# Optimization experiments

Hardware: AMD Instinct MI355X
Metric: run time of the kernel (lower is better)

The kernel has to match this reference:

```python
import jax, jax.numpy as jnp
import numpy as np
jax.config.update('jax_enable_x64', True)

H = 16          # tree height -> n = 2**H
TP = 16         # parallel coordinate dims
F = 2
DIV = 2
K = F * H // DIV          # 16
N = 1 << H                # 65536
EMB = 1_000_000
T = 2048                  # rows in this block


def setup_inputs() -> dict:
    key = jax.random.key(0)
    k1, k2, k3 = jax.random.split(key, 3)
    # location table: signed ints in [1-n, n), as in torch.randint(1-n, n, ...)
    locations = jax.random.randint(k1, (EMB, TP), 1 - N, N, dtype=jnp.int64)
    pos_idx = jax.random.randint(k2, (T,), 0, EMB, dtype=jnp.int64)
    norm = jax.random.uniform(k3, (T, 1, 1), dtype=jnp.float32)
    return {"locations": locations, "pos_idx": pos_idx, "norm": norm}


def _generate_random_masks(key, sz):
    # masks[i] uniform in [0, 2**i) per level i  (note: & binds looser than -,
    # so torch code computes rand & (2**i - 1))
    upper = (jnp.int64(1) << jnp.arange(H, dtype=jnp.int64)) - 1  # (H,)
    rn = jax.random.randint(key, (H, sz, K, TP), 0, N, dtype=jnp.int64)
    masks = rn & upper[:, None, None, None]
    return jnp.transpose(masks, (1, 0, 2, 3))  # (sz, H, K, TP)


def _connection(key, ori_int):
    # ori_int: (T, TP) int64
    kmask, kperm = jax.random.split(key)
    flip_masks = (jnp.int64(1) << jnp.arange(H, dtype=jnp.int64))[None, :, None]  # (1,H,1)
    flipped = ori_int[:, None, :] ^ flip_masks                    # (T, H, TP)
    rmasks = _generate_random_masks(kmask, flipped.shape[0])      # (T, H, K, TP)
    result = (flipped[:, :, None, :] ^ rmasks).reshape(T, H * K, TP)
    loc = jnp.concatenate([result, ori_int[:, None, :], -result], axis=1)  # (T, 2HK+1, TP)
    perm = jax.random.permutation(kperm, loc.shape[1])
    return loc[:, perm, :]


def _distance(coord1, coord2, norm):
    # sign product: +1 if same sign (>=0 vs <0), else -1
    sg = (jnp.where(coord1 >= 0, 1.0, -1.0) * jnp.where(coord2 >= 0, 1.0, -1.0)).astype(jnp.float32)
    xor = jnp.abs(coord1) ^ jnp.abs(coord2)
    _, e = jnp.frexp((xor + 1).astype(jnp.float32))  # frexp exponent == bit length
    s = e.astype(jnp.float32) / H
    return sg * (1.0 - s) * norm


def reference(locations, pos_idx, norm):
    # gather this block's node locations (irregular gather from large table)
    ori = locations[pos_idx]                         # (T, TP)
    key = jax.random.key(42)
    loc = _connection(key, ori)                      # (T, 2HK+1, TP) candidate neighbors
    # distances from each candidate back to the original location
    return _distance(loc, ori[:, None, :], norm)     # (T, 2HK+1, TP) float32
```

## Files before the change

### kernel.cpp

```cpp
#include <hip/hip_runtime.h>
#include <stdint.h>


#define H_   16
#define TP_  16
#define K_   16
#define T_   2048
#define NC   513

typedef float f32x4 __attribute__((ext_vector_type(4)));

struct TFPair { uint32_t a, b; };

__host__ __device__ constexpr uint32_t rotl32(uint32_t x, int r) {
  return (x << r) | (x >> (32 - r));
}

__host__ __device__ constexpr TFPair tf2x32(uint32_t k0, uint32_t k1,
                                            uint32_t x0, uint32_t x1) {
  uint32_t ks0 = k0, ks1 = k1, ks2 = k0 ^ k1 ^ 0x1BD11BDAu;
  x0 += ks0; x1 += ks1;
  x0 += x1; x1 = rotl32(x1, 13); x1 ^= x0;
  x0 += x1; x1 = rotl32(x1, 15); x1 ^= x0;
  x0 += x1; x1 = rotl32(x1, 26); x1 ^= x0;
  x0 += x1; x1 = rotl32(x1,  6); x1 ^= x0;
  x0 += ks1; x1 += ks2 + 1u;
  x0 += x1; x1 = rotl32(x1, 17); x1 ^= x0;
  x0 += x1; x1 = rotl32(x1, 29); x1 ^= x0;
  x0 += x1; x1 = rotl32(x1, 16); x1 ^= x0;
  x0 += x1; x1 = rotl32(x1, 24); x1 ^= x0;
  x0 += ks2; x1 += ks0 + 2u;
  x0 += x1; x1 = rotl32(x1, 13); x1 ^= x0;
  x0 += x1; x1 = rotl32(x1, 15); x1 ^= x0;
  x0 += x1; x1 = rotl32(x1, 26); x1 ^= x0;
  x0 += x1; x1 = rotl32(x1,  6); x1 ^= x0;
  x0 += ks0; x1 += ks1 + 3u;
  x0 += x1; x1 = rotl32(x1, 17); x1 ^= x0;
  x0 += x1; x1 = rotl32(x1, 29); x1 ^= x0;
  x0 += x1; x1 = rotl32(x1, 16); x1 ^= x0;
  x0 += x1; x1 = rotl32(x1, 24); x1 ^= x0;
  x0 += ks1; x1 += ks2 + 4u;
  x0 += x1; x1 = rotl32(x1, 13); x1 ^= x0;
  x0 += x1; x1 = rotl32(x1, 15); x1 ^= x0;
  x0 += x1; x1 = rotl32(x1, 26); x1 ^= x0;
  x0 += x1; x1 = rotl32(x1,  6); x1 ^= x0;
  x0 += ks2; x1 += ks0 + 5u;
  return {x0, x1};
}

constexpr TFPair KM = tf2x32(0u, 42u, 0u, 0u);
constexpr TFPair KP = tf2x32(0u, 42u, 0u, 1u);
constexpr TFPair C2 = tf2x32(KM.a, KM.b, 0u, 1u);
constexpr uint32_t KLO0 = C2.a, KLO1 = C2.b;
constexpr TFPair SB = tf2x32(KP.a, KP.b, 0u, 1u);
constexpr uint32_t KSUB0 = SB.a, KSUB1 = SB.b;

struct Keys { uint32_t v[NC]; };
constexpr Keys make_keys() {
  Keys k{};
  for (int i = 0; i < NC; ++i) {
    TFPair r = tf2x32(KSUB0, KSUB1, 0u, (uint32_t)i);
    k.v[i] = r.a ^ r.b;
  }
  return k;
}
constexpr Keys KEYS = make_keys();

#define PART_SZ 33
struct Part { int v[PART_SZ]; };
constexpr Part make_part(int lo) {
  Part p{};
  for (int m = lo; m < lo + PART_SZ && m < NC; ++m) {
    uint32_t km = KEYS.v[m];
    int rank = 0;
    for (int j = 0; j < NC; ++j) {
      uint32_t kj = KEYS.v[j];
      if (kj < km || (kj == km && j < m)) ++rank;
    }
    p.v[m - lo] = rank;
  }
  return p;
}
constexpr Part PT0  = make_part(0),   PT1  = make_part(33),
               PT2  = make_part(66),  PT3  = make_part(99),
               PT4  = make_part(132), PT5  = make_part(165),
               PT6  = make_part(198), PT7  = make_part(231),
               PT8  = make_part(264), PT9  = make_part(297),
               PT10 = make_part(330), PT11 = make_part(363),
               PT12 = make_part(396), PT13 = make_part(429),
               PT14 = make_part(462), PT15 = make_part(495);

struct IPerm { int v[NC]; };
constexpr IPerm merge_parts() {
  IPerm r{};
  const Part* ps[16] = {&PT0, &PT1, &PT2,  &PT3,  &PT4,  &PT5,  &PT6,  &PT7,
                        &PT8, &PT9, &PT10, &PT11, &PT12, &PT13, &PT14, &PT15};
  for (int c = 0; c < 16; ++c)
    for (int i = 0; i < PART_SZ; ++i) {
      int m = c * PART_SZ + i;
      if (m < NC) r.v[m] = ps[c]->v[i];
    }
  return r;
}
constexpr IPerm IPERM = merge_parts();
constexpr int C_ORI = IPERM.v[256];

struct CTab { uint32_t v[256]; };
constexpr CTab make_ctab() {
  CTab c{};
  for (int j = 0; j < 256; ++j)
    c.v[j] = (uint32_t)IPERM.v[j] | ((uint32_t)IPERM.v[j + 257] << 16);
  return c;
}
constexpr CTab CTAB = make_ctab();
__device__ __constant__ CTab d_ctab = CTAB;

__global__ __launch_bounds__(256, 4) void dist_kernel(
    const int* __restrict__ locations, const int* __restrict__ pos_idx,
    const float* __restrict__ norm, float* __restrict__ out) {
  __shared__ __align__(16) float buf[NC * TP_];

  const int t   = (int)blockIdx.x;
  const int tid = (int)threadIdx.x;
  const int tp  = tid & 15;
  const int jl  = tid >> 4;

  const int   ori  = locations[pos_idx[t] * TP_ + tp];
  const float nm   = norm[t];
  const float nm16 = nm * 0.0625f;

  if (tid < 16) buf[C_ORI * TP_ + tid] = 0.9375f * nm;

  uint32_t ct[16];
#pragma unroll
  for (int i = 0; i < 16; ++i) ct[i] = d_ctab.v[(jl << 4) + i];

  const uint32_t flip_h = 1u << jl;
  const uint32_t mask_h = flip_h - 1u;
  const uint32_t base   = (uint32_t)(((jl * T_ + t) * K_) * TP_ + tp);
  const uint32_t ao     = (uint32_t)(ori < 0 ? -ori : ori);

#pragma unroll
  for (int jj = 0; jj < 16; ++jj) {
    const TFPair r = tf2x32(KLO0, KLO1, 0u, base + (uint32_t)(jj * TP_));
    const uint32_t fm = flip_h ^ (r.b & mask_h);
    const int v = ori ^ (int)fm;

    const uint32_t sgbit = ((uint32_t)(v ^ ori)) & 0x80000000u;
    const uint32_t av = (uint32_t)(v < 0 ? -v : v);
    const uint32_t x  = (av ^ ao) + 1u;
    const int e = 32 - __clz((int)x);
    const float f  = nm - (float)e * nm16;
    const float d1 = __uint_as_float(__float_as_uint(f) ^ sgbit);
    const float d2 = (v == 0) ? d1
                   : __uint_as_float(__float_as_uint(d1) ^ 0x80000000u);

    const uint32_t pr = ct[jj];
    buf[(pr & 0xffffu) * TP_ + tp] = d1;
    buf[(pr >> 16)     * TP_ + tp] = d2;
  }

  __syncthreads();

  const f32x4* __restrict__ b4 = (const f32x4*)buf;
  f32x4* __restrict__ o4 = (f32x4*)(out + (size_t)t * (NC * TP_));
#pragma unroll
  for (int it = 0; it < 8; ++it)
    __builtin_nontemporal_store(b4[(it << 8) + tid], o4 + (it << 8) + tid);
  if (tid < 4)
    __builtin_nontemporal_store(b4[2048 + tid], o4 + 2048 + tid);
}

extern "C" void kernel_launch(void* const* d_in, const int* in_sizes, int n_in,
                              void* d_out, int out_size, void* d_ws, size_t ws_size,
                              hipStream_t stream) {
  const int*   locations = (const int*)d_in[0];
  const int*   pos_idx   = (const int*)d_in[1];
  const float* norm      = (const float*)d_in[2];
  float* out = (float*)d_out;

  hipLaunchKernelGGL(dist_kernel, dim3(T_), dim3(256), 0, stream,
                     locations, pos_idx, norm, out);
}
```

Baseline: 116.9 us.

## Process four rows per block with prefetched gathers and manual barriers

Each block now handles four consecutive rows instead of one. The grid shrinks to a quarter, the constant permutation table loads are amortized across rows, and the next row's location gather and norm are prefetched while the current row computes. Barriers use explicit lgkmcnt waits and sched_barriers so the global stores are not forced to drain before the next row starts writing shared memory. In exchange the grid has fewer blocks (512 for 256 CUs), the rows inside a block are serialized, and the block-level parallelism that hid store latency is reduced.

```diff
diff --git a/kernel.cpp b/kernel.cpp
--- a/kernel.cpp
+++ b/kernel.cpp
@@ -7,6 +7,8 @@
 #define K_   16
 #define T_   2048
 #define NC   513
+#define ROWS 4
+#define GRID (T_ / ROWS)
 
 typedef float f32x4 __attribute__((ext_vector_type(4)));
 
@@ -120,16 +122,10 @@
     const float* __restrict__ norm, float* __restrict__ out) {
   __shared__ __align__(16) float buf[NC * TP_];
 
-  const int t   = (int)blockIdx.x;
   const int tid = (int)threadIdx.x;
   const int tp  = tid & 15;
   const int jl  = tid >> 4;
-
-  const int   ori  = locations[pos_idx[t] * TP_ + tp];
-  const float nm   = norm[t];
-  const float nm16 = nm * 0.0625f;
-
-  if (tid < 16) buf[C_ORI * TP_ + tid] = 0.9375f * nm;
+  const int t0  = (int)blockIdx.x * ROWS;
 
   uint32_t ct[16];
 #pragma unroll
@@ -137,38 +133,68 @@
 
   const uint32_t flip_h = 1u << jl;
   const uint32_t mask_h = flip_h - 1u;
-  const uint32_t base   = (uint32_t)(((jl * T_ + t) * K_) * TP_ + tp);
-  const uint32_t ao     = (uint32_t)(ori < 0 ? -ori : ori);
+  const f32x4* __restrict__ b4 = (const f32x4*)buf;
+
+  int   ori_c = locations[pos_idx[t0] * TP_ + tp];
+  float nm_c  = norm[t0];
+
+#pragma unroll 1
+  for (int row = 0; row < ROWS; ++row) {
+    const int t = t0 + row;
+
+    int ori_n = 0; float nm_n = 0.0f;
+    if (row + 1 < ROWS) {
+      ori_n = locations[pos_idx[t + 1] * TP_ + tp];
+      nm_n  = norm[t + 1];
+    }
+
+    const int   ori  = ori_c;
+    const float nm   = nm_c;
+    const float nm16 = nm * 0.0625f;
+    const uint32_t ao   = (uint32_t)(ori < 0 ? -ori : ori);
+    const uint32_t base = (uint32_t)(((jl * T_ + t) * K_) * TP_ + tp);
+
+    if (tid < 16) buf[C_ORI * TP_ + tid] = 0.9375f * nm;
 
 #pragma unroll
-  for (int jj = 0; jj < 16; ++jj) {
-    const TFPair r = tf2x32(KLO0, KLO1, 0u, base + (uint32_t)(jj * TP_));
-    const uint32_t fm = flip_h ^ (r.b & mask_h);
-    const int v = ori ^ (int)fm;
-
-    const uint32_t sgbit = ((uint32_t)(v ^ ori)) & 0x80000000u;
-    const uint32_t av = (uint32_t)(v < 0 ? -v : v);
-    const uint32_t x  = (av ^ ao) + 1u;
-    const int e = 32 - __clz((int)x);
-    const float f  = nm - (float)e * nm16;
-    const float d1 = __uint_as_float(__float_as_uint(f) ^ sgbit);
-    const float d2 = (v == 0) ? d1
-                   : __uint_as_float(__float_as_uint(d1) ^ 0x80000000u);
-
-    const uint32_t pr = ct[jj];
-    buf[(pr & 0xffffu) * TP_ + tp] = d1;
-    buf[(pr >> 16)     * TP_ + tp] = d2;
+    for (int jj = 0; jj < 16; ++jj) {
+      const TFPair r = tf2x32(KLO0, KLO1, 0u, base + (uint32_t)(jj * TP_));
+      const uint32_t fm = flip_h ^ (r.b & mask_h);
+      const int v = ori ^ (int)fm;
+
+      const uint32_t sgbit = ((uint32_t)(v ^ ori)) & 0x80000000u;
+      const uint32_t av = (uint32_t)(v < 0 ? -v : v);
+      const uint32_t x  = (av ^ ao) + 1u;
+      const int e = 32 - __clz((int)x);
+      const float f  = nm - (float)e * nm16;
+      const float d1 = __uint_as_float(__float_as_uint(f) ^ sgbit);
+      const float d2 = (v == 0) ? d1
+                     : __uint_as_float(__float_as_uint(d1) ^ 0x80000000u);
+
+      const uint32_t pr = ct[jj];
+      buf[(pr & 0xffffu) * TP_ + tp] = d1;
+      buf[(pr >> 16)     * TP_ + tp] = d2;
+    }
+
+    __builtin_amdgcn_sched_barrier(0);
+    asm volatile("s_waitcnt lgkmcnt(0)" ::: "memory");
+    __builtin_amdgcn_s_barrier();
+    __builtin_amdgcn_sched_barrier(0);
+
+    f32x4* __restrict__ o4 = (f32x4*)(out + (size_t)t * (NC * TP_));
+#pragma unroll
+    for (int it = 0; it < 8; ++it)
+      __builtin_nontemporal_store(b4[(it << 8) + tid], o4 + (it << 8) + tid);
+    if (tid < 4)
+      __builtin_nontemporal_store(b4[2048 + tid], o4 + 2048 + tid);
+
+    __builtin_amdgcn_sched_barrier(0);
+    asm volatile("" ::: "memory");
+    __builtin_amdgcn_s_barrier();
+    __builtin_amdgcn_sched_barrier(0);
+
+    ori_c = ori_n; nm_c = nm_n;
   }
-
-  __syncthreads();
-
-  const f32x4* __restrict__ b4 = (const f32x4*)buf;
-  f32x4* __restrict__ o4 = (f32x4*)(out + (size_t)t * (NC * TP_));
-#pragma unroll
-  for (int it = 0; it < 8; ++it)
-    __builtin_nontemporal_store(b4[(it << 8) + tid], o4 + (it << 8) + tid);
-  if (tid < 4)
-    __builtin_nontemporal_store(b4[2048 + tid], o4 + 2048 + tid);
 }
 
 extern "C" void kernel_launch(void* const* d_in, const int* in_sizes, int n_in,
@@ -179,6 +205,6 @@
   const float* norm      = (const float*)d_in[2];
   float* out = (float*)d_out;
 
-  hipLaunchKernelGGL(dist_kernel, dim3(T_), dim3(256), 0, stream,
+  hipLaunchKernelGGL(dist_kernel, dim3(GRID), dim3(256), 0, stream,
                      locations, pos_idx, norm, out);
 }
```

Measured after the change: 118.0 us. Within noise of the previous version (+0.9%).
